# Kernel optimization log

Hardware: AMD Instinct MI355X
Metric: run time of the kernel (lower is better)

The kernel has to match this reference:

```python
import jax, jax.numpy as jnp
import numpy as np

STU_NUM, ITEM_NUM, CONC_NUM, EMB_DIM, BATCH = 20000, 8000, 128, 32, 128


def setup_inputs() -> dict:
    key = jax.random.key(0)
    ks = jax.random.split(key, 12)
    # 1-based student ids, as in the original (forward does stu - 1)
    stu_list = jax.random.randint(ks[0], (BATCH,), 1, STU_NUM + 1, dtype=jnp.int32)
    stu_emb = jax.random.normal(ks[1], (STU_NUM, EMB_DIM), jnp.float32)
    item_emb = jax.random.normal(ks[2], (ITEM_NUM, EMB_DIM), jnp.float32)
    disc = jax.random.normal(ks[3], (ITEM_NUM, 1), jnp.float32)
    # binary Q-matrix (item x concept), float as in Q.float()
    Q = (jax.random.uniform(ks[4], (ITEM_NUM, CONC_NUM)) < 0.3).astype(jnp.float32)
    # emb2conc: Linear(emb_dim, conc_num) + sigmoid
    w1 = jax.random.normal(ks[5], (CONC_NUM, EMB_DIM), jnp.float32) / np.sqrt(EMB_DIM)
    b1 = jax.random.normal(ks[6], (CONC_NUM,), jnp.float32) * 0.1
    # pred_layer: Linear(conc_num, 1) + sigmoid
    wp = jax.random.normal(ks[7], (1, CONC_NUM), jnp.float32) / np.sqrt(CONC_NUM)
    bp = jax.random.normal(ks[8], (1,), jnp.float32) * 0.1
    gw_stu = jax.random.normal(ks[9], (STU_NUM, 1), jnp.float32)
    gw_Q = jax.random.normal(ks[10], (CONC_NUM, 1), jnp.float32)
    # guess_adju_layer2: Linear(1,1) + sigmoid
    w2 = jax.random.normal(ks[11], (1, 1), jnp.float32)
    b2 = jnp.zeros((1,), jnp.float32)
    return {"stu_list": stu_list, "stu_emb": stu_emb, "item_emb": item_emb,
            "disc": disc, "Q": Q, "w1": w1, "b1": b1, "wp": wp, "bp": bp,
            "gw_stu": gw_stu, "gw_Q": gw_Q, "w2": w2, "b2": b2}


def reference(stu_list, stu_emb, item_emb, disc, Q, w1, b1, wp, bp, gw_stu, gw_Q, w2, b2):
    idx = stu_list - 1                                        # 1-based -> 0-based
    stu_conc = jax.nn.sigmoid(stu_emb[idx] @ w1.T + b1)       # [B, C]
    item_conc = jax.nn.sigmoid(item_emb @ w1.T + b1)          # [I, C]
    # X = Q * (stu_emb_conc - item_emb_conc) * disc, batched over students
    X = Q[None, :, :] * (stu_conc[:, None, :] - item_conc[None, :, :]) * disc[None, :, :]  # [B, I, C]
    P = jax.nn.sigmoid(jnp.einsum('bic,c->bi', X, wp[0]) + bp[0])   # [B, I]
    Q_adju = (Q @ gw_Q)[:, 0]                                 # [I]
    g1 = jax.nn.sigmoid(gw_stu[idx] + Q_adju[None, :])        # [B,1]+[1,I] -> [B, I]
    g2 = jax.nn.sigmoid(g1 * w2[0, 0] + b2[0])                # Linear(1,1)+sigmoid
    return g2 + (1.0 - g2) * P                                # [B, I]
```

## Files before the change

### kernel.cpp

```cpp
#include <hip/hip_runtime.h>
#include <hip/hip_bf16.h>

#define ITEM 8000
#define CONC 128
#define EMB  32
#define BATCH 128
#define NBLK 500
#define IB   16
#define SE_S 56
#define SC_S 136

typedef short s16x8 __attribute__((ext_vector_type(8)));
typedef float f32x4 __attribute__((ext_vector_type(4)));

__device__ __forceinline__ float sigmoidf(float x) { return 1.f / (1.f + __expf(-x)); }
__device__ __forceinline__ short f2bf(float x) {
    __hip_bfloat16 h = __float2bfloat16(x);
    return *reinterpret_cast<short*>(&h);
}
__device__ __forceinline__ void cvt16(const float4* __restrict__ src, short* dst) {
    float4 f0 = src[0], f1 = src[1], f2 = src[2], f3 = src[3];
    s16x8 a, b;
    a[0]=f2bf(f0.x); a[1]=f2bf(f0.y); a[2]=f2bf(f0.z); a[3]=f2bf(f0.w);
    a[4]=f2bf(f1.x); a[5]=f2bf(f1.y); a[6]=f2bf(f1.z); a[7]=f2bf(f1.w);
    b[0]=f2bf(f2.x); b[1]=f2bf(f2.y); b[2]=f2bf(f2.z); b[3]=f2bf(f2.w);
    b[4]=f2bf(f3.x); b[5]=f2bf(f3.y); b[6]=f2bf(f3.z); b[7]=f2bf(f3.w);
    *(s16x8*)dst = a;
    *(s16x8*)(dst + 8) = b;
}

__global__ __launch_bounds__(256) void fused_kernel(
    const int* __restrict__ stu_list, const float* __restrict__ stu_emb,
    const float* __restrict__ item_emb, const float* __restrict__ disc,
    const float* __restrict__ Q, const float* __restrict__ w1,
    const float* __restrict__ b1, const float* __restrict__ wp,
    const float* __restrict__ bp_, const float* __restrict__ gw_stu,
    const float* __restrict__ gw_Q, const float* __restrict__ w2,
    const float* __restrict__ b2, float* __restrict__ out)
{
    __shared__ __align__(16) short sembL[BATCH * SE_S];
    __shared__ __align__(16) short w1L  [CONC * SE_S];
    __shared__ __align__(16) short itembL[IB * SE_S];
    __shared__ __align__(16) short scbL [BATCH * SC_S];
    __shared__ __align__(16) short qwL  [IB * SC_S];
    __shared__ float ptT[4][IB], ptQ[4][IB], gsL[BATCH];

    const int tid = threadIdx.x;
    const int i0  = blockIdx.x * IB;
    const int w   = tid >> 6;
    const int lane = tid & 63;
    const int l15 = lane & 15, lk = lane >> 4;

    {
        int row = tid >> 1, half = tid & 1;
        int sid = stu_list[row] - 1;
        cvt16((const float4*)(stu_emb + (size_t)sid * EMB + half * 16),
              &sembL[row * SE_S + half * 16]);
        cvt16((const float4*)(w1 + row * EMB + half * 16),
              &w1L[row * SE_S + half * 16]);
        if (tid < 2 * IB) {
            int ir = tid >> 1, ih = tid & 1;
            cvt16((const float4*)(item_emb + (size_t)(i0 + ir) * EMB + ih * 16),
                  &itembL[ir * SE_S + ih * 16]);
        }
        if (tid < BATCH) gsL[tid] = gw_stu[stu_list[tid] - 1];
    }
    __syncthreads();

    {
        s16x8 af0 = *(const s16x8*)&sembL[((2 * w + 0) * 16 + l15) * SE_S + lk * 8];
        s16x8 af1 = *(const s16x8*)&sembL[((2 * w + 1) * 16 + l15) * SE_S + lk * 8];
#pragma unroll
        for (int ct = 0; ct < 8; ++ct) {
            s16x8 bf = *(const s16x8*)&w1L[(ct * 16 + l15) * SE_S + lk * 8];
            int c = ct * 16 + l15;
            float bc = b1[c];
            f32x4 z = {0.f, 0.f, 0.f, 0.f};
            f32x4 d0 = __builtin_amdgcn_mfma_f32_16x16x32_bf16(af0, bf, z, 0, 0, 0);
            f32x4 d1 = __builtin_amdgcn_mfma_f32_16x16x32_bf16(af1, bf, z, 0, 0, 0);
#pragma unroll
            for (int r = 0; r < 4; ++r) {
                scbL[((2 * w + 0) * 16 + lk * 4 + r) * SC_S + c] = f2bf(sigmoidf(d0[r] + bc) - 0.5f);
                scbL[((2 * w + 1) * 16 + lk * 4 + r) * SC_S + c] = f2bf(sigmoidf(d1[r] + bc) - 0.5f);
            }
        }
    }

    {
        s16x8 iaf = *(const s16x8*)&itembL[l15 * SE_S + lk * 8];
        float at[4] = {0.f, 0.f, 0.f, 0.f}, aq[4] = {0.f, 0.f, 0.f, 0.f};
#pragma unroll
        for (int j = 0; j < 2; ++j) {
            int ct = 2 * w + j;
            int c  = ct * 16 + l15;
            s16x8 bf = *(const s16x8*)&w1L[(ct * 16 + l15) * SE_S + lk * 8];
            f32x4 z = {0.f, 0.f, 0.f, 0.f};
            f32x4 d = __builtin_amdgcn_mfma_f32_16x16x32_bf16(iaf, bf, z, 0, 0, 0);
            float bc = b1[c], wpc = wp[c], gqc = gw_Q[c];
#pragma unroll
            for (int r = 0; r < 4; ++r) {
                int it = lk * 4 + r;
                float ic = sigmoidf(d[r] + bc);
                float q  = Q[(size_t)(i0 + it) * CONC + c];
                float u  = q * wpc;
                qwL[it * SC_S + c] = f2bf(u);
                at[r] += u * (ic - 0.5f);
                aq[r] += q * gqc;
            }
        }
#pragma unroll
        for (int off = 1; off < 16; off <<= 1) {
#pragma unroll
            for (int r = 0; r < 4; ++r) {
                at[r] += __shfl_xor(at[r], off);
                aq[r] += __shfl_xor(aq[r], off);
            }
        }
        if (l15 == 0) {
#pragma unroll
            for (int r = 0; r < 4; ++r) { ptT[w][lk * 4 + r] = at[r]; ptQ[w][lk * 4 + r] = aq[r]; }
        }
    }
    __syncthreads();

    {
        s16x8 bfr[4];
#pragma unroll
        for (int ks = 0; ks < 4; ++ks)
            bfr[ks] = *(const s16x8*)&qwL[l15 * SC_S + ks * 32 + lk * 8];

        const int i = i0 + l15;
        const float di = disc[i];
        const float ti = ptT[0][l15] + ptT[1][l15] + ptT[2][l15] + ptT[3][l15];
        const float qi = ptQ[0][l15] + ptQ[1][l15] + ptQ[2][l15] + ptQ[3][l15];
        const float W2 = w2[0], B2 = b2[0], BP = bp_[0];
#pragma unroll
        for (int j = 0; j < 2; ++j) {
            const int bt = 2 * w + j;
            f32x4 acc = {0.f, 0.f, 0.f, 0.f};
#pragma unroll
            for (int ks = 0; ks < 4; ++ks) {
                s16x8 af = *(const s16x8*)&scbL[(bt * 16 + l15) * SC_S + ks * 32 + lk * 8];
                acc = __builtin_amdgcn_mfma_f32_16x16x32_bf16(af, bfr[ks], acc, 0, 0, 0);
            }
#pragma unroll
            for (int r = 0; r < 4; ++r) {
                int b = bt * 16 + lk * 4 + r;
                float P  = sigmoidf(di * (acc[r] - ti) + BP);
                float g1 = sigmoidf(gsL[b] + qi);
                float g2 = sigmoidf(fmaf(g1, W2, B2));
                out[(size_t)b * ITEM + i] = g2 + (1.f - g2) * P;
            }
        }
    }
}

extern "C" void kernel_launch(void* const* d_in, const int* in_sizes, int n_in,
                              void* d_out, int out_size, void* d_ws, size_t ws_size,
                              hipStream_t stream) {
    const int*   stu_list = (const int*)d_in[0];
    const float* stu_emb  = (const float*)d_in[1];
    const float* item_emb = (const float*)d_in[2];
    const float* disc     = (const float*)d_in[3];
    const float* Q        = (const float*)d_in[4];
    const float* w1       = (const float*)d_in[5];
    const float* b1       = (const float*)d_in[6];
    const float* wp       = (const float*)d_in[7];
    const float* bp       = (const float*)d_in[8];
    const float* gw_stu   = (const float*)d_in[9];
    const float* gw_Q     = (const float*)d_in[10];
    const float* w2       = (const float*)d_in[11];
    const float* b2       = (const float*)d_in[12];
    float* out = (float*)d_out;

    fused_kernel<<<NBLK, 256, 0, stream>>>(stu_list, stu_emb, item_emb, disc, Q,
                                           w1, b1, wp, bp, gw_stu, gw_Q, w2, b2, out);
}
```

Baseline: 92.20 us.

## Double item tile to 32 per block with 512 threads, halving redundant per-block setup

Each block now covers 32 items with 8 waves instead of 16 items with 4 waves, so the grid is halved to 250 blocks. The per-block recomputation of student concept activations (128x128 sigmoid GEMM) and the w1/student embedding conversion are amortised over twice as many items. Work is remapped so each wave owns one 16-student tile and loops over two item tiles. The trade-off is fewer blocks than CUs on the device, which may leave some compute units idle and cut latency hiding for the output stores.

```diff
diff --git a/kernel.cpp b/kernel.cpp
--- a/kernel.cpp
+++ b/kernel.cpp
@@ -5,8 +5,8 @@
 #define CONC 128
 #define EMB  32
 #define BATCH 128
-#define NBLK 500
-#define IB   16
+#define IB   32
+#define NBLK 250
 #define SE_S 56
 #define SC_S 136
 
@@ -29,7 +29,7 @@
     *(s16x8*)(dst + 8) = b;
 }
 
-__global__ __launch_bounds__(256) void fused_kernel(
+__global__ __launch_bounds__(512) void fused_kernel(
     const int* __restrict__ stu_list, const float* __restrict__ stu_emb,
     const float* __restrict__ item_emb, const float* __restrict__ disc,
     const float* __restrict__ Q, const float* __restrict__ w1,
@@ -43,7 +43,7 @@
     __shared__ __align__(16) short itembL[IB * SE_S];
     __shared__ __align__(16) short scbL [BATCH * SC_S];
     __shared__ __align__(16) short qwL  [IB * SC_S];
-    __shared__ float ptT[4][IB], ptQ[4][IB], gsL[BATCH];
+    __shared__ float ptT[8][IB], ptQ[8][IB], gsL[BATCH];
 
     const int tid = threadIdx.x;
     const int i0  = blockIdx.x * IB;
@@ -52,12 +52,15 @@
     const int l15 = lane & 15, lk = lane >> 4;
 
     {
-        int row = tid >> 1, half = tid & 1;
-        int sid = stu_list[row] - 1;
-        cvt16((const float4*)(stu_emb + (size_t)sid * EMB + half * 16),
-              &sembL[row * SE_S + half * 16]);
-        cvt16((const float4*)(w1 + row * EMB + half * 16),
-              &w1L[row * SE_S + half * 16]);
+        int r2 = (tid & 255) >> 1, half = tid & 1;
+        if (tid < 256) {
+            int sid = stu_list[r2] - 1;
+            cvt16((const float4*)(stu_emb + (size_t)sid * EMB + half * 16),
+                  &sembL[r2 * SE_S + half * 16]);
+        } else {
+            cvt16((const float4*)(w1 + r2 * EMB + half * 16),
+                  &w1L[r2 * SE_S + half * 16]);
+        }
         if (tid < 2 * IB) {
             int ir = tid >> 1, ih = tid & 1;
             cvt16((const float4*)(item_emb + (size_t)(i0 + ir) * EMB + ih * 16),
@@ -68,84 +71,87 @@
     __syncthreads();
 
     {
-        s16x8 af0 = *(const s16x8*)&sembL[((2 * w + 0) * 16 + l15) * SE_S + lk * 8];
-        s16x8 af1 = *(const s16x8*)&sembL[((2 * w + 1) * 16 + l15) * SE_S + lk * 8];
+        s16x8 af = *(const s16x8*)&sembL[(w * 16 + l15) * SE_S + lk * 8];
 #pragma unroll
         for (int ct = 0; ct < 8; ++ct) {
             s16x8 bf = *(const s16x8*)&w1L[(ct * 16 + l15) * SE_S + lk * 8];
             int c = ct * 16 + l15;
             float bc = b1[c];
             f32x4 z = {0.f, 0.f, 0.f, 0.f};
-            f32x4 d0 = __builtin_amdgcn_mfma_f32_16x16x32_bf16(af0, bf, z, 0, 0, 0);
-            f32x4 d1 = __builtin_amdgcn_mfma_f32_16x16x32_bf16(af1, bf, z, 0, 0, 0);
+            f32x4 d = __builtin_amdgcn_mfma_f32_16x16x32_bf16(af, bf, z, 0, 0, 0);
 #pragma unroll
-            for (int r = 0; r < 4; ++r) {
-                scbL[((2 * w + 0) * 16 + lk * 4 + r) * SC_S + c] = f2bf(sigmoidf(d0[r] + bc) - 0.5f);
-                scbL[((2 * w + 1) * 16 + lk * 4 + r) * SC_S + c] = f2bf(sigmoidf(d1[r] + bc) - 0.5f);
-            }
+            for (int r = 0; r < 4; ++r)
+                scbL[(w * 16 + lk * 4 + r) * SC_S + c] = f2bf(sigmoidf(d[r] + bc) - 0.5f);
         }
     }
 
     {
-        s16x8 iaf = *(const s16x8*)&itembL[l15 * SE_S + lk * 8];
-        float at[4] = {0.f, 0.f, 0.f, 0.f}, aq[4] = {0.f, 0.f, 0.f, 0.f};
+        s16x8 ia0 = *(const s16x8*)&itembL[l15 * SE_S + lk * 8];
+        s16x8 ia1 = *(const s16x8*)&itembL[(16 + l15) * SE_S + lk * 8];
+        s16x8 bf  = *(const s16x8*)&w1L[(w * 16 + l15) * SE_S + lk * 8];
+        const int c = w * 16 + l15;
+        const float bc = b1[c], wpc = wp[c], gqc = gw_Q[c];
+        f32x4 z = {0.f, 0.f, 0.f, 0.f};
+        f32x4 d0 = __builtin_amdgcn_mfma_f32_16x16x32_bf16(ia0, bf, z, 0, 0, 0);
+        f32x4 d1 = __builtin_amdgcn_mfma_f32_16x16x32_bf16(ia1, bf, z, 0, 0, 0);
+        float at[8], aq[8];
 #pragma unroll
         for (int j = 0; j < 2; ++j) {
-            int ct = 2 * w + j;
-            int c  = ct * 16 + l15;
-            s16x8 bf = *(const s16x8*)&w1L[(ct * 16 + l15) * SE_S + lk * 8];
-            f32x4 z = {0.f, 0.f, 0.f, 0.f};
-            f32x4 d = __builtin_amdgcn_mfma_f32_16x16x32_bf16(iaf, bf, z, 0, 0, 0);
-            float bc = b1[c], wpc = wp[c], gqc = gw_Q[c];
 #pragma unroll
             for (int r = 0; r < 4; ++r) {
-                int it = lk * 4 + r;
-                float ic = sigmoidf(d[r] + bc);
+                int it = j * 16 + lk * 4 + r;
+                float dv = (j ? d1[r] : d0[r]);
+                float ic = sigmoidf(dv + bc);
                 float q  = Q[(size_t)(i0 + it) * CONC + c];
                 float u  = q * wpc;
                 qwL[it * SC_S + c] = f2bf(u);
-                at[r] += u * (ic - 0.5f);
-                aq[r] += q * gqc;
+                at[j * 4 + r] = u * (ic - 0.5f);
+                aq[j * 4 + r] = q * gqc;
             }
         }
 #pragma unroll
         for (int off = 1; off < 16; off <<= 1) {
 #pragma unroll
-            for (int r = 0; r < 4; ++r) {
-                at[r] += __shfl_xor(at[r], off);
-                aq[r] += __shfl_xor(aq[r], off);
+            for (int k = 0; k < 8; ++k) {
+                at[k] += __shfl_xor(at[k], off);
+                aq[k] += __shfl_xor(aq[k], off);
             }
         }
         if (l15 == 0) {
 #pragma unroll
-            for (int r = 0; r < 4; ++r) { ptT[w][lk * 4 + r] = at[r]; ptQ[w][lk * 4 + r] = aq[r]; }
+            for (int k = 0; k < 8; ++k) {
+                int it = (k >> 2) * 16 + lk * 4 + (k & 3);
+                ptT[w][it] = at[k];
+                ptQ[w][it] = aq[k];
+            }
         }
     }
     __syncthreads();
 
     {
-        s16x8 bfr[4];
+        s16x8 af[4];
 #pragma unroll
         for (int ks = 0; ks < 4; ++ks)
-            bfr[ks] = *(const s16x8*)&qwL[l15 * SC_S + ks * 32 + lk * 8];
+            af[ks] = *(const s16x8*)&scbL[(w * 16 + l15) * SC_S + ks * 32 + lk * 8];
 
-        const int i = i0 + l15;
-        const float di = disc[i];
-        const float ti = ptT[0][l15] + ptT[1][l15] + ptT[2][l15] + ptT[3][l15];
-        const float qi = ptQ[0][l15] + ptQ[1][l15] + ptQ[2][l15] + ptQ[3][l15];
         const float W2 = w2[0], B2 = b2[0], BP = bp_[0];
 #pragma unroll
         for (int j = 0; j < 2; ++j) {
-            const int bt = 2 * w + j;
             f32x4 acc = {0.f, 0.f, 0.f, 0.f};
 #pragma unroll
             for (int ks = 0; ks < 4; ++ks) {
-                s16x8 af = *(const s16x8*)&scbL[(bt * 16 + l15) * SC_S + ks * 32 + lk * 8];
-                acc = __builtin_amdgcn_mfma_f32_16x16x32_bf16(af, bfr[ks], acc, 0, 0, 0);
+                s16x8 bfr = *(const s16x8*)&qwL[(j * 16 + l15) * SC_S + ks * 32 + lk * 8];
+                acc = __builtin_amdgcn_mfma_f32_16x16x32_bf16(af[ks], bfr, acc, 0, 0, 0);
             }
+            const int il = j * 16 + l15;
+            const int i  = i0 + il;
+            const float di = disc[i];
+            float ti = 0.f, qi = 0.f;
+#pragma unroll
+            for (int w8 = 0; w8 < 8; ++w8) { ti += ptT[w8][il]; qi += ptQ[w8][il]; }
 #pragma unroll
             for (int r = 0; r < 4; ++r) {
-                int b = bt * 16 + lk * 4 + r;
+                int b = w * 16 + lk * 4 + r;
                 float P  = sigmoidf(di * (acc[r] - ti) + BP);
                 float g1 = sigmoidf(gsL[b] + qi);
                 float g2 = sigmoidf(fmaf(g1, W2, B2));
@@ -173,6 +179,6 @@
     const float* b2       = (const float*)d_in[12];
     float* out = (float*)d_out;
 
-    fused_kernel<<<NBLK, 256, 0, stream>>>(stu_list, stu_emb, item_emb, disc, Q,
+    fused_kernel<<<NBLK, 512, 0, stream>>>(stu_list, stu_emb, item_emb, disc, Q,
                                            w1, b1, wp, bp, gw_stu, gw_Q, w2, b2, out);
 }
```

Measured after the change: 90.89 us. No clear change (-1.4%).
